# Optimization experiments

Measured on AMD Instinct MI355X. Metric: run time of the kernel, lower is better.

Reference implementation:

```python
import jax, jax.numpy as jnp
import numpy as np

N_SAMPLES = 2097152
FEAT_DIM = 16
HIDDEN = 64


def sh_deg4(d):
    # tcnn SphericalHarmonics degree 4 basis (16 outputs).
    # tcnn internally maps input in [0,1] back to [-1,1] via 2*x-1; the module
    # feeds (dirs+1)/2, so the basis is evaluated on the raw (reflected) dirs.
    x, y, z = d[..., 0], d[..., 1], d[..., 2]
    xy, xz, yz = x * y, x * z, y * z
    x2, y2, z2 = x * x, y * y, z * z
    return jnp.stack([
        jnp.full_like(x, 0.28209479177387814),
        -0.48860251190291987 * y,
        0.48860251190291987 * z,
        -0.48860251190291987 * x,
        1.0925484305920792 * xy,
        -1.0925484305920792 * yz,
        0.94617469575755997 * z2 - 0.31539156525251999,
        -1.0925484305920792 * xz,
        0.54627421529603959 * (x2 - y2),
        0.59004358992664352 * y * (-3.0 * x2 + y2),
        2.8906114426405538 * xy * z,
        0.45704579946446572 * y * (1.0 - 5.0 * z2),
        0.3731763325901154 * z * (5.0 * z2 - 3.0),
        0.45704579946446572 * x * (1.0 - 5.0 * z2),
        1.4453057213202769 * z * (x2 - y2),
        0.59004358992664352 * x * (-x2 + 3.0 * y2),
    ], axis=-1)


def _unit(k, shape):
    v = jax.random.normal(k, shape, dtype=jnp.float32)
    return v / jnp.linalg.norm(v, axis=-1, keepdims=True)


def setup_inputs() -> dict:
    key = jax.random.key(0)
    ks = jax.random.split(key, 6)
    in_dim = FEAT_DIM + 16 + 3  # features + SH(deg4) + normals = 35
    return {
        "features": jax.random.normal(ks[0], (N_SAMPLES, FEAT_DIM), dtype=jnp.float32),
        "dirs": _unit(ks[1], (N_SAMPLES, 3)),
        "normals": _unit(ks[2], (N_SAMPLES, 3)),
        "W1": jax.random.normal(ks[3], (in_dim, HIDDEN), dtype=jnp.float32) / np.sqrt(in_dim),
        "W2": jax.random.normal(ks[4], (HIDDEN, HIDDEN), dtype=jnp.float32) / np.sqrt(HIDDEN),
        "W3": jax.random.normal(ks[5], (HIDDEN, 3), dtype=jnp.float32) / np.sqrt(HIDDEN),
    }


def reference(features, dirs, normals, W1, W2, W3):
    # reflect view dirs about the surface normal
    refl = dirs - 2.0 * jnp.sum(dirs * normals, axis=-1, keepdims=True) * normals
    # module does (d+1)/2 then tcnn SH (which undoes it) -> SH on refl directly
    dirs_embd = sh_deg4(refl)
    inp = jnp.concatenate([features, dirs_embd, normals], axis=-1)  # [N, 35]
    h = jax.nn.relu(inp @ W1)
    h = jax.nn.relu(h @ W2)
    color = (h @ W3).astype(jnp.float32)
    return jax.nn.sigmoid(color)  # color_activation = sigmoid
```

## Files before the change

kernel.cpp:

```cpp
#include <hip/hip_runtime.h>
#include <hip/hip_bf16.h>
#include <math.h>

#define NS 2097152
#define NGROUP (NS / 16)
#define NBLOCK 1024
#define NWAVES (NBLOCK * 4)

typedef __attribute__((ext_vector_type(8))) short bf16x8;
typedef __attribute__((ext_vector_type(4))) float f32x4;

union FragU { unsigned u[4]; bf16x8 v; };

__device__ __forceinline__ unsigned pkbf16(float lo, float hi) {
    union { __hip_bfloat162 h; unsigned u; } cv;
    cv.h = __halves2bfloat162(__float2bfloat16(lo), __float2bfloat16(hi));
    return cv.u;
}

__device__ __forceinline__ float sigmoidf_(float x) {
    return 1.0f / (1.0f + expf(-x));
}

__global__ __launch_bounds__(256, 2) void radiance_mfma_kernel(
    const float* __restrict__ features,
    const float* __restrict__ dirs,
    const float* __restrict__ normals,
    const float* __restrict__ W1,
    const float* __restrict__ W2,
    const float* __restrict__ W3,
    float* __restrict__ out)
{
    __shared__ __align__(16) unsigned char lds[4][4096];

    const int tid  = threadIdx.x;
    const int wid  = tid >> 6;
    const int lane = tid & 63;
    const int s    = lane & 15;
    const int hi   = lane >> 4;
    const int wave_id = blockIdx.x * 4 + wid;

    unsigned char* wb  = &lds[wid][0];
    unsigned char* wb2 = wb + 2048;
    const unsigned sw = (unsigned)((s & 7) << 4);

    const f32x4 zero = {0.f, 0.f, 0.f, 0.f};

    bf16x8 a1[4][2], a2[4][2], a3[2];

    #pragma unroll
    for (int t = 0; t < 4; ++t) {
        #pragma unroll
        for (int st = 0; st < 2; ++st) {
            FragU q;
            #pragma unroll
            for (int d = 0; d < 4; ++d) {
                int k0 = st * 32 + hi * 8 + 2 * d;
                int k1 = k0 + 1;
                int m  = t * 16 + s;
                float w0 = (k0 < 35) ? W1[k0 * 64 + m] : 0.f;
                float w1 = (k1 < 35) ? W1[k1 * 64 + m] : 0.f;
                q.u[d] = pkbf16(w0, w1);
            }
            a1[t][st] = q.v;
        }
    }
    #pragma unroll
    for (int t = 0; t < 4; ++t) {
        #pragma unroll
        for (int st = 0; st < 2; ++st) {
            FragU q;
            #pragma unroll
            for (int d = 0; d < 4; ++d) {
                int k0 = st * 32 + hi * 8 + 2 * d;
                int m  = t * 16 + s;
                q.u[d] = pkbf16(W2[k0 * 64 + m], W2[(k0 + 1) * 64 + m]);
            }
            a2[t][st] = q.v;
        }
    }
    #pragma unroll
    for (int st = 0; st < 2; ++st) {
        FragU q;
        #pragma unroll
        for (int d = 0; d < 4; ++d) {
            int k0 = st * 32 + hi * 8 + 2 * d;
            float w0 = (s < 3) ? W3[k0 * 3 + s] : 0.f;
            float w1 = (s < 3) ? W3[(k0 + 1) * 3 + s] : 0.f;
            q.u[d] = pkbf16(w0, w1);
        }
        a3[st] = q.v;
    }

    for (int g = wave_id; g < NGROUP; g += NWAVES) {
        const size_t smp = (size_t)g * 16 + s;

        unsigned u0, u1, u2, u3, v0, v1, v2, v3;
        if (hi < 2) {
            const float* fb = features + smp * 16 + (size_t)hi * 8;
            float4 fA = *(const float4*)fb;
            float4 fB = *(const float4*)(fb + 4);
            u0 = pkbf16(fA.x, fA.y); u1 = pkbf16(fA.z, fA.w);
            u2 = pkbf16(fB.x, fB.y); u3 = pkbf16(fB.z, fB.w);
            if (hi == 0) {
                const float* np = normals + smp * 3;
                float nx = np[0], ny = np[1], nz = np[2];
                v0 = pkbf16(nx, ny); v1 = pkbf16(nz, 0.f); v2 = 0; v3 = 0;
            } else {
                v0 = v1 = v2 = v3 = 0;
            }
        } else {
            const float* dp = dirs + smp * 3;
            const float* np = normals + smp * 3;
            float dx = dp[0], dy = dp[1], dz = dp[2];
            float nx = np[0], ny = np[1], nz = np[2];
            float dn = dx * nx + dy * ny + dz * nz;
            float m2 = -2.0f * dn;
            float x = fmaf(m2, nx, dx);
            float y = fmaf(m2, ny, dy);
            float z = fmaf(m2, nz, dz);
            float xy = x * y, xz = x * z, yz = y * z;
            float x2 = x * x, y2 = y * y, z2 = z * z;
            float sh0 = 0.28209479177387814f;
            float sh1 = -0.48860251190291987f * y;
            float sh2 =  0.48860251190291987f * z;
            float sh3 = -0.48860251190291987f * x;
            float sh4 =  1.0925484305920792f * xy;
            float sh5 = -1.0925484305920792f * yz;
            float sh6 = fmaf(0.94617469575755997f, z2, -0.31539156525251999f);
            float sh7 = -1.0925484305920792f * xz;
            float sh8  = 0.54627421529603959f * (x2 - y2);
            float sh9  = 0.59004358992664352f * y * fmaf(-3.0f, x2, y2);
            float sh10 = 2.8906114426405538f * xy * z;
            float sh11 = 0.45704579946446572f * y * fmaf(-5.0f, z2, 1.0f);
            float sh12 = 0.3731763325901154f * z * fmaf(5.0f, z2, -3.0f);
            float sh13 = 0.45704579946446572f * x * fmaf(-5.0f, z2, 1.0f);
            float sh14 = 1.4453057213202769f * z * (x2 - y2);
            float sh15 = 0.59004358992664352f * x * fmaf(-1.0f, x2, 3.0f * y2);
            unsigned e0 = pkbf16(sh0, sh1),  e1 = pkbf16(sh2, sh3);
            unsigned e2 = pkbf16(sh4, sh5),  e3 = pkbf16(sh6, sh7);
            unsigned f0 = pkbf16(sh8, sh9),  f1 = pkbf16(sh10, sh11);
            unsigned f2 = pkbf16(sh12, sh13), f3 = pkbf16(sh14, sh15);
            bool odd = (hi & 1);
            u0 = odd ? f0 : e0; u1 = odd ? f1 : e1;
            u2 = odd ? f2 : e2; u3 = odd ? f3 : e3;
            v0 = v1 = v2 = v3 = 0;
        }
        bf16x8 B0, B1v;
        { FragU q; q.u[0] = u0; q.u[1] = u1; q.u[2] = u2; q.u[3] = u3; B0 = q.v; }
        { FragU q; q.u[0] = v0; q.u[1] = v1; q.u[2] = v2; q.u[3] = v3; B1v = q.v; }

        f32x4 acc1[4];
        #pragma unroll
        for (int t = 0; t < 4; ++t)
            acc1[t] = __builtin_amdgcn_mfma_f32_16x16x32_bf16(a1[t][0], B0, zero, 0, 0, 0);
        #pragma unroll
        for (int t = 0; t < 4; ++t)
            acc1[t] = __builtin_amdgcn_mfma_f32_16x16x32_bf16(a1[t][1], B1v, acc1[t], 0, 0, 0);

        #pragma unroll
        for (int t = 0; t < 4; ++t) {
            float h0 = fmaxf(acc1[t][0], 0.f), h1_ = fmaxf(acc1[t][1], 0.f);
            float h2_ = fmaxf(acc1[t][2], 0.f), h3_ = fmaxf(acc1[t][3], 0.f);
            unsigned base = (unsigned)(s * 128 + (t * 16 + hi * 4) * 2);
            *(unsigned*)(wb + (base ^ sw))       = pkbf16(h0, h1_);
            *(unsigned*)(wb + ((base + 4) ^ sw)) = pkbf16(h2_, h3_);
        }

        bf16x8 hB[2];
        #pragma unroll
        for (int st = 0; st < 2; ++st)
            hB[st] = *(const bf16x8*)(wb + (((unsigned)(s * 128 + st * 64 + hi * 16)) ^ sw));

        f32x4 acc2[4];
        #pragma unroll
        for (int t = 0; t < 4; ++t)
            acc2[t] = __builtin_amdgcn_mfma_f32_16x16x32_bf16(a2[t][0], hB[0], zero, 0, 0, 0);
        #pragma unroll
        for (int t = 0; t < 4; ++t)
            acc2[t] = __builtin_amdgcn_mfma_f32_16x16x32_bf16(a2[t][1], hB[1], acc2[t], 0, 0, 0);

        #pragma unroll
        for (int t = 0; t < 4; ++t) {
            float h0 = fmaxf(acc2[t][0], 0.f), h1_ = fmaxf(acc2[t][1], 0.f);
            float h2_ = fmaxf(acc2[t][2], 0.f), h3_ = fmaxf(acc2[t][3], 0.f);
            unsigned base = (unsigned)(s * 128 + (t * 16 + hi * 4) * 2);
            *(unsigned*)(wb2 + (base ^ sw))       = pkbf16(h0, h1_);
            *(unsigned*)(wb2 + ((base + 4) ^ sw)) = pkbf16(h2_, h3_);
        }

        bf16x8 hC[2];
        #pragma unroll
        for (int st = 0; st < 2; ++st)
            hC[st] = *(const bf16x8*)(wb2 + (((unsigned)(s * 128 + st * 64 + hi * 16)) ^ sw));

        f32x4 acc3 = __builtin_amdgcn_mfma_f32_16x16x32_bf16(a3[0], hC[0], zero, 0, 0, 0);
        acc3 = __builtin_amdgcn_mfma_f32_16x16x32_bf16(a3[1], hC[1], acc3, 0, 0, 0);

        float o0 = sigmoidf_(acc3[0]);
        float o1 = sigmoidf_(acc3[1]);
        float o2 = sigmoidf_(acc3[2]);
        if (hi == 0) {
            float* ob = out + ((size_t)g * 16 + s) * 3;
            ob[0] = o0; ob[1] = o1; ob[2] = o2;
        }
    }
}

extern "C" void kernel_launch(void* const* d_in, const int* in_sizes, int n_in,
                              void* d_out, int out_size, void* d_ws, size_t ws_size,
                              hipStream_t stream) {
    const float* features = (const float*)d_in[0];
    const float* dirs     = (const float*)d_in[1];
    const float* normals  = (const float*)d_in[2];
    const float* W1       = (const float*)d_in[3];
    const float* W2       = (const float*)d_in[4];
    const float* W3       = (const float*)d_in[5];
    float* out = (float*)d_out;

    radiance_mfma_kernel<<<NBLOCK, 256, 0, stream>>>(
        features, dirs, normals, W1, W2, W3, out);
}
```

Baseline: 326.9 us.

## Software-prefetch next group's inputs, precompute LDS offsets, use fast sigmoid

Restructures the grid-stride loop into a fixed-trip-count loop that loads the next group's features, dirs and normals into registers while the current group's MLP runs, so global-load latency overlaps the MFMA work. LDS write and read offsets are precomputed once, and the paired 32-bit stores become single 64-bit stores. Sigmoid now uses fast __expf and __fdividef. Launch bounds rise to 4 waves per SIMD, which tightens the register budget while the prefetch buffers add register pressure.

```diff
diff --git a/kernel.cpp b/kernel.cpp
--- a/kernel.cpp
+++ b/kernel.cpp
@@ -6,6 +6,7 @@
 #define NGROUP (NS / 16)
 #define NBLOCK 1024
 #define NWAVES (NBLOCK * 4)
+#define ITERS (NGROUP / NWAVES)
 
 typedef __attribute__((ext_vector_type(8))) short bf16x8;
 typedef __attribute__((ext_vector_type(4))) float f32x4;
@@ -18,11 +19,7 @@
     return cv.u;
 }
 
-__device__ __forceinline__ float sigmoidf_(float x) {
-    return 1.0f / (1.0f + expf(-x));
-}
-
-__global__ __launch_bounds__(256, 2) void radiance_mfma_kernel(
+__global__ __launch_bounds__(256, 4) void radiance_mfma2_kernel(
     const float* __restrict__ features,
     const float* __restrict__ dirs,
     const float* __restrict__ normals,
@@ -45,6 +42,14 @@
     const unsigned sw = (unsigned)((s & 7) << 4);
 
     const f32x4 zero = {0.f, 0.f, 0.f, 0.f};
+
+    unsigned wof[4], rof[2];
+    #pragma unroll
+    for (int t = 0; t < 4; ++t)
+        wof[t] = ((unsigned)(s * 128 + t * 32 + hi * 8)) ^ sw;
+    #pragma unroll
+    for (int st = 0; st < 2; ++st)
+        rof[st] = ((unsigned)(s * 128 + st * 64 + hi * 16)) ^ sw;
 
     bf16x8 a1[4][2], a2[4][2], a3[2];
 
@@ -92,33 +97,51 @@
         a3[st] = q.v;
     }
 
-    for (int g = wave_id; g < NGROUP; g += NWAVES) {
-        const size_t smp = (size_t)g * 16 + s;
-
-        unsigned u0, u1, u2, u3, v0, v1, v2, v3;
+    float4 cfA, cfB;
+    float cdx, cdy, cdz, cnx, cny, cnz;
+    {
+        unsigned smp = (unsigned)wave_id * 16u + (unsigned)s;
         if (hi < 2) {
-            const float* fb = features + smp * 16 + (size_t)hi * 8;
-            float4 fA = *(const float4*)fb;
-            float4 fB = *(const float4*)(fb + 4);
-            u0 = pkbf16(fA.x, fA.y); u1 = pkbf16(fA.z, fA.w);
-            u2 = pkbf16(fB.x, fB.y); u3 = pkbf16(fB.z, fB.w);
+            const float* fb = features + (size_t)smp * 16 + hi * 8;
+            cfA = *(const float4*)fb;
+            cfB = *(const float4*)(fb + 4);
             if (hi == 0) {
-                const float* np = normals + smp * 3;
-                float nx = np[0], ny = np[1], nz = np[2];
-                v0 = pkbf16(nx, ny); v1 = pkbf16(nz, 0.f); v2 = 0; v3 = 0;
-            } else {
-                v0 = v1 = v2 = v3 = 0;
+                const float* np = normals + (size_t)smp * 3;
+                cnx = np[0]; cny = np[1]; cnz = np[2];
             }
         } else {
-            const float* dp = dirs + smp * 3;
-            const float* np = normals + smp * 3;
-            float dx = dp[0], dy = dp[1], dz = dp[2];
-            float nx = np[0], ny = np[1], nz = np[2];
-            float dn = dx * nx + dy * ny + dz * nz;
+            const float* dp = dirs + (size_t)smp * 3;
+            const float* np = normals + (size_t)smp * 3;
+            cdx = dp[0]; cdy = dp[1]; cdz = dp[2];
+            cnx = np[0]; cny = np[1]; cnz = np[2];
+        }
+    }
+
+    unsigned g = (unsigned)wave_id;
+    #pragma unroll 1
+    for (int it = 0; it < ITERS; ++it) {
+        const unsigned gn   = (it == ITERS - 1) ? g : g + (unsigned)NWAVES;
+        const unsigned smpn = gn * 16u + (unsigned)s;
+
+        unsigned u0, u1, u2, u3, v0, v1;
+        if (hi < 2) {
+            u0 = pkbf16(cfA.x, cfA.y); u1 = pkbf16(cfA.z, cfA.w);
+            u2 = pkbf16(cfB.x, cfB.y); u3 = pkbf16(cfB.z, cfB.w);
+            if (hi == 0) { v0 = pkbf16(cnx, cny); v1 = pkbf16(cnz, 0.f); }
+            else         { v0 = 0; v1 = 0; }
+            const float* fb = features + (size_t)smpn * 16 + hi * 8;
+            cfA = *(const float4*)fb;
+            cfB = *(const float4*)(fb + 4);
+            if (hi == 0) {
+                const float* np = normals + (size_t)smpn * 3;
+                cnx = np[0]; cny = np[1]; cnz = np[2];
+            }
+        } else {
+            float dn = cdx * cnx + cdy * cny + cdz * cnz;
             float m2 = -2.0f * dn;
-            float x = fmaf(m2, nx, dx);
-            float y = fmaf(m2, ny, dy);
-            float z = fmaf(m2, nz, dz);
+            float x = fmaf(m2, cnx, cdx);
+            float y = fmaf(m2, cny, cdy);
+            float z = fmaf(m2, cnz, cdz);
             float xy = x * y, xz = x * z, yz = y * z;
             float x2 = x * x, y2 = y * y, z2 = z * z;
             float sh0 = 0.28209479177387814f;
@@ -144,11 +167,15 @@
             bool odd = (hi & 1);
             u0 = odd ? f0 : e0; u1 = odd ? f1 : e1;
             u2 = odd ? f2 : e2; u3 = odd ? f3 : e3;
-            v0 = v1 = v2 = v3 = 0;
+            v0 = 0; v1 = 0;
+            const float* dp = dirs + (size_t)smpn * 3;
+            const float* np = normals + (size_t)smpn * 3;
+            cdx = dp[0]; cdy = dp[1]; cdz = dp[2];
+            cnx = np[0]; cny = np[1]; cnz = np[2];
         }
         bf16x8 B0, B1v;
         { FragU q; q.u[0] = u0; q.u[1] = u1; q.u[2] = u2; q.u[3] = u3; B0 = q.v; }
-        { FragU q; q.u[0] = v0; q.u[1] = v1; q.u[2] = v2; q.u[3] = v3; B1v = q.v; }
+        { FragU q; q.u[0] = v0; q.u[1] = v1; q.u[2] = 0;  q.u[3] = 0;  B1v = q.v; }
 
         f32x4 acc1[4];
         #pragma unroll
@@ -160,50 +187,43 @@
 
         #pragma unroll
         for (int t = 0; t < 4; ++t) {
-            float h0 = fmaxf(acc1[t][0], 0.f), h1_ = fmaxf(acc1[t][1], 0.f);
-            float h2_ = fmaxf(acc1[t][2], 0.f), h3_ = fmaxf(acc1[t][3], 0.f);
-            unsigned base = (unsigned)(s * 128 + (t * 16 + hi * 4) * 2);
-            *(unsigned*)(wb + (base ^ sw))       = pkbf16(h0, h1_);
-            *(unsigned*)(wb + ((base + 4) ^ sw)) = pkbf16(h2_, h3_);
-        }
-
-        bf16x8 hB[2];
-        #pragma unroll
-        for (int st = 0; st < 2; ++st)
-            hB[st] = *(const bf16x8*)(wb + (((unsigned)(s * 128 + st * 64 + hi * 16)) ^ sw));
+            uint2 w;
+            w.x = pkbf16(fmaxf(acc1[t][0], 0.f), fmaxf(acc1[t][1], 0.f));
+            w.y = pkbf16(fmaxf(acc1[t][2], 0.f), fmaxf(acc1[t][3], 0.f));
+            *(uint2*)(wb + wof[t]) = w;
+        }
+        bf16x8 hB0 = *(const bf16x8*)(wb + rof[0]);
+        bf16x8 hB1 = *(const bf16x8*)(wb + rof[1]);
 
         f32x4 acc2[4];
         #pragma unroll
         for (int t = 0; t < 4; ++t)
-            acc2[t] = __builtin_amdgcn_mfma_f32_16x16x32_bf16(a2[t][0], hB[0], zero, 0, 0, 0);
-        #pragma unroll
-        for (int t = 0; t < 4; ++t)
-            acc2[t] = __builtin_amdgcn_mfma_f32_16x16x32_bf16(a2[t][1], hB[1], acc2[t], 0, 0, 0);
+            acc2[t] = __builtin_amdgcn_mfma_f32_16x16x32_bf16(a2[t][0], hB0, zero, 0, 0, 0);
+        #pragma unroll
+        for (int t = 0; t < 4; ++t)
+            acc2[t] = __builtin_amdgcn_mfma_f32_16x16x32_bf16(a2[t][1], hB1, acc2[t], 0, 0, 0);
 
         #pragma unroll
         for (int t = 0; t < 4; ++t) {
-            float h0 = fmaxf(acc2[t][0], 0.f), h1_ = fmaxf(acc2[t][1], 0.f);
-            float h2_ = fmaxf(acc2[t][2], 0.f), h3_ = fmaxf(acc2[t][3], 0.f);
-            unsigned base = (unsigned)(s * 128 + (t * 16 + hi * 4) * 2);
-            *(unsigned*)(wb2 + (base ^ sw))       = pkbf16(h0, h1_);
-            *(unsigned*)(wb2 + ((base + 4) ^ sw)) = pkbf16(h2_, h3_);
-        }
-
-        bf16x8 hC[2];
-        #pragma unroll
-        for (int st = 0; st < 2; ++st)
-            hC[st] = *(const bf16x8*)(wb2 + (((unsigned)(s * 128 + st * 64 + hi * 16)) ^ sw));
-
-        f32x4 acc3 = __builtin_amdgcn_mfma_f32_16x16x32_bf16(a3[0], hC[0], zero, 0, 0, 0);
-        acc3 = __builtin_amdgcn_mfma_f32_16x16x32_bf16(a3[1], hC[1], acc3, 0, 0, 0);
-
-        float o0 = sigmoidf_(acc3[0]);
-        float o1 = sigmoidf_(acc3[1]);
-        float o2 = sigmoidf_(acc3[2]);
+            uint2 w;
+            w.x = pkbf16(fmaxf(acc2[t][0], 0.f), fmaxf(acc2[t][1], 0.f));
+            w.y = pkbf16(fmaxf(acc2[t][2], 0.f), fmaxf(acc2[t][3], 0.f));
+            *(uint2*)(wb2 + wof[t]) = w;
+        }
+        bf16x8 hC0 = *(const bf16x8*)(wb2 + rof[0]);
+        bf16x8 hC1 = *(const bf16x8*)(wb2 + rof[1]);
+
+        f32x4 acc3 = __builtin_amdgcn_mfma_f32_16x16x32_bf16(a3[0], hC0, zero, 0, 0, 0);
+        acc3 = __builtin_amdgcn_mfma_f32_16x16x32_bf16(a3[1], hC1, acc3, 0, 0, 0);
+
+        float o0 = __fdividef(1.0f, 1.0f + __expf(-acc3[0]));
+        float o1 = __fdividef(1.0f, 1.0f + __expf(-acc3[1]));
+        float o2 = __fdividef(1.0f, 1.0f + __expf(-acc3[2]));
         if (hi == 0) {
-            float* ob = out + ((size_t)g * 16 + s) * 3;
+            float* ob = out + (size_t)(g * 16u + (unsigned)s) * 3;
             ob[0] = o0; ob[1] = o1; ob[2] = o2;
         }
+        g = gn;
     }
 }
 
@@ -218,6 +238,6 @@
     const float* W3       = (const float*)d_in[5];
     float* out = (float*)d_out;
 
-    radiance_mfma_kernel<<<NBLOCK, 256, 0, stream>>>(
+    radiance_mfma2_kernel<<<NBLOCK, 256, 0, stream>>>(
         features, dirs, normals, W1, W2, W3, out);
 }
```

After: 314.3 us. 1.04x faster.
